# Performance work log

Hardware: AMD Instinct MI355X
Metric: run time of the kernel (lower is better)

## Reference

```python
import jax, jax.numpy as jnp
import numpy as np
from jax import lax

K = 31  # neighborhood kernel size
HEADS = 4


def nat2d(x, qkv_w, qkv_b, rpb, proj_w, proj_b, heads=HEADS, k=K):
    """Neighborhood Attention 2D. x: (B,H,W,C) NHWC. Returns (B,H,W,C)."""
    B, H, W, C = x.shape
    dh = C // heads
    scale = dh ** -0.5
    K2 = k * k
    qkv = x @ qkv_w.T + qkv_b                      # (B,H,W,3C)
    qkv = qkv.reshape(B, H, W, 3, heads, dh)
    q, kk, v = qkv[..., 0, :, :], qkv[..., 1, :, :], qkv[..., 2, :, :]
    # neighborhood window start, clamped to image (NATTEN semantics)
    ri = jnp.clip(jnp.arange(H) - k // 2, 0, H - k)   # (H,)
    ci = jnp.clip(jnp.arange(W) - k // 2, 0, W - k)   # (W,)
    row_idx = ri[:, None] + jnp.arange(k)[None, :]    # (H,k)
    col_idx = ci[:, None] + jnp.arange(k)[None, :]    # (W,k)

    def gather(t):  # (B,H,W,heads,dh) -> (B,H,W,K2,heads,dh)
        g = t[:, row_idx]                  # (B,H,k,W,heads,dh)
        g = g[:, :, :, col_idx]            # (B,H,k,W,k,heads,dh)
        g = jnp.transpose(g, (0, 1, 3, 2, 4, 5, 6))
        return g.reshape(B, H, W, K2, heads, dh)

    kg = gather(kk)
    vg = gather(v)
    logits = jnp.einsum('bijhd,bijnhd->bijhn', q * scale, kg)  # (B,H,W,heads,K2)
    # relative position bias: rpb (heads, 2k-1, 2k-1), index = key - query + (k-1)
    rrel = row_idx - jnp.arange(H)[:, None] + (k - 1)  # (H,k)
    crel = col_idx - jnp.arange(W)[:, None] + (k - 1)  # (W,k)
    bias = rpb[:, rrel]                                # (heads,H,k,2k-1)
    bias = bias[:, :, :, crel]                         # (heads,H,k,W,k)
    bias = jnp.transpose(bias, (0, 1, 3, 2, 4)).reshape(heads, H, W, K2)
    logits = logits + jnp.transpose(bias, (1, 2, 0, 3))[None]
    attn = jax.nn.softmax(logits, axis=-1)
    out = jnp.einsum('bijhn,bijnhd->bijhd', attn, vg).reshape(B, H, W, C)
    return out @ proj_w.T + proj_b


def setup_inputs() -> dict:
    key = jax.random.key(0)
    ks = jax.random.split(key, 16)
    B, H, W, C = 1, 36, 36, 64
    s = 0.02
    inp = {
        'x': jax.random.normal(ks[0], (B, H * W, C), jnp.float32),
        'H': H, 'W': W,
        'qkv_w1': jax.random.normal(ks[1], (3 * C, C), jnp.float32) * s,
        'qkv_b1': jnp.zeros((3 * C,), jnp.float32),
        'rpb1': jax.random.normal(ks[2], (HEADS, 2 * K - 1, 2 * K - 1), jnp.float32) * s,
        'proj_w1': jax.random.normal(ks[3], (C, C), jnp.float32) * s,
        'proj_b1': jnp.zeros((C,), jnp.float32),
        'qkv_w2': jax.random.normal(ks[4], (3 * C, C), jnp.float32) * s,
        'qkv_b2': jnp.zeros((3 * C,), jnp.float32),
        'rpb2': jax.random.normal(ks[5], (HEADS, 2 * K - 1, 2 * K - 1), jnp.float32) * s,
        'proj_w2': jax.random.normal(ks[6], (C, C), jnp.float32) * s,
        'proj_b2': jnp.zeros((C,), jnp.float32),
        'dw_w': jax.random.normal(ks[7], (C, 1, 3, 3), jnp.float32) * s,
        'dw_b': jnp.zeros((C,), jnp.float32),
        'lin_w': jax.random.normal(ks[8], (C, C), jnp.float32) * s,
        'lin_b': jnp.zeros((C,), jnp.float32),
    }
    return inp


def reference(x, H, W, qkv_w1, qkv_b1, rpb1, proj_w1, proj_b1,
              qkv_w2, qkv_b2, rpb2, proj_w2, proj_b2,
              dw_w, dw_b, lin_w, lin_b):
    B, N, C = x.shape
    x_nhwc = x.reshape(B, H, W, C)
    x_nat = nat2d(x_nhwc, qkv_w1, qkv_b1, rpb1, proj_w1, proj_b1)
    x_nat = nat2d(x_nat, qkv_w2, qkv_b2, rpb2, proj_w2, proj_b2)
    x_bchw = jnp.transpose(x_nhwc, (0, 3, 1, 2))
    x_conv = lax.conv_general_dilated(
        x_bchw, dw_w, window_strides=(1, 1), padding=((1, 1), (1, 1)),
        feature_group_count=C,
        dimension_numbers=('NCHW', 'OIHW', 'NCHW')) + dw_b[None, :, None, None]
    out = jnp.transpose(x_nat, (0, 3, 1, 2)) + x_conv       # (B,C,H,W)
    out = out.reshape(B, C, H * W).transpose(0, 2, 1)        # (B,L,C)
    return out @ lin_w.T + lin_b
```

## Files before the change

### kernel.cpp

```cpp
#include <hip/hip_runtime.h>


namespace {

__device__ __forceinline__ int iclampi(int v, int lo, int hi) {
  return v < lo ? lo : (v > hi ? hi : v);
}

template <bool WITH_T>
__global__ __launch_bounds__(256) void qkv_fused(
    const float* __restrict__ xin, const float* __restrict__ w,
    const float* __restrict__ b, float* __restrict__ planes,
    const float* __restrict__ pw1, const float* __restrict__ pw2,
    const float* __restrict__ lw, float* __restrict__ wT) {
  const int bid = blockIdx.x;
  const int tid = threadIdx.x;
  if (WITH_T && bid >= 1008) {
    const int t = bid - 1008;
    const int m = t >> 4;
    const int idx = (t & 15) * 256 + tid;
    const float* src = m == 0 ? pw1 : (m == 1 ? pw2 : lw);
    wT[m * 4096 + (idx & 63) * 64 + (idx >> 6)] = src[idx];
    return;
  }
  __shared__ float xs[64][65];
  __shared__ float ws4[4][64];
  const int pg = bid % 21, rg = bid / 21;
  const int wv = tid >> 6, lane = tid & 63;
  const int n0 = pg * 64;
  const int base = n0 * 64;
  const int maxf = 82944 - base;
  const float* xb = xin + base;
#pragma unroll
  for (int t4 = 0; t4 < 4; ++t4) {
    const int fi = (tid + t4 * 256) * 4;
    float4 v = make_float4(0.f, 0.f, 0.f, 0.f);
    if (fi < maxf) v = *(const float4*)(xb + fi);
    const int p = fi >> 6, c = fi & 63;
    xs[p][c] = v.x; xs[p][c + 1] = v.y; xs[p][c + 2] = v.z; xs[p][c + 3] = v.w;
  }
  ws4[tid >> 6][tid & 63] = w[rg * 256 + tid];
  __syncthreads();
  const int r = rg * 4 + wv;
  float acc = b[r];
#pragma unroll
  for (int cc = 0; cc < 64; ++cc) acc += xs[lane][cc] * ws4[wv][cc];
  const int n = n0 + lane;
  if (n < 1296) planes[r * 1296 + n] = acc;
}

__global__ __launch_bounds__(256, 2) void nat_attn_part(
    const float* __restrict__ planes, const float* __restrict__ rpb,
    float* __restrict__ part) {
  __shared__ float lpart[4][16][35];

  const int tid = threadIdx.x;
  const int h = tid >> 6;
  const int lane = tid & 63;
  const int bid = blockIdx.x;
  const int tile = bid >> 3;
  const int s = (bid >> 1) & 3;
  const int pr = bid & 1;
  const int i0 = (tile / 18) * 2;
  const int j0 = (tile % 18) * 2;

  const int r_lo = iclampi(i0 - 15, 0, 5);
  const int nRr = (iclampi(i0 - 14, 0, 5) + 30) - r_lo;
  const int c_lo = iclampi(j0 - 15, 0, 5);
  const int nCc = (iclampi(j0 - 14, 0, 5) + 30) - c_lo;

  const int iq = i0 + pr;
  const int riq = iclampi(iq - 15, 0, 5);
  int jq[2], cjq[2];
#pragma unroll
  for (int qq = 0; qq < 2; ++qq) {
    jq[qq] = j0 + qq;
    cjq[qq] = iclampi(jq[qq] - 15, 0, 5);
  }

  const float* Qp = planes + (size_t)(h * 16) * 1296;
  const float* Kp = planes + (size_t)(64 + h * 16) * 1296;
  const float* Vp = planes + (size_t)(128 + h * 16) * 1296;

  float qv[2][16];
#pragma unroll
  for (int qq = 0; qq < 2; ++qq) {
    const int nq = iq * 36 + jq[qq];
#pragma unroll
    for (int d = 0; d < 16; ++d) qv[qq][d] = Qp[d * 1296 + nq] * 0.25f;
  }

  float acc[2][16];
  float sden[2] = {0.f, 0.f};
#pragma unroll
  for (int qq = 0; qq < 2; ++qq)
#pragma unroll
    for (int d = 0; d < 16; ++d) acc[qq][d] = 0.f;

  const int lr = lane >> 5;
  const int lc = lane & 31;

#pragma unroll
  for (int rp = 0; rp < 4; ++rp) {
    const int krr = s * 8 + rp * 2 + lr;
    const int rA = r_lo + krr;
    const int cA = c_lo + lc;
    const bool act = (krr <= nRr) && (lc <= nCc);
    const int rL = rA > 35 ? 35 : rA;
    const int cL = cA > 35 ? 35 : cA;
    const int nk = rL * 36 + cL;
    float kr_[16], vr_[16];
#pragma unroll
    for (int d = 0; d < 16; ++d) kr_[d] = Kp[d * 1296 + nk];
#pragma unroll
    for (int d = 0; d < 16; ++d) vr_[d] = Vp[d * 1296 + nk];

    float dot[2] = {0.f, 0.f};
#pragma unroll
    for (int d = 0; d < 16; ++d) {
      dot[0] += qv[0][d] * kr_[d];
      dot[1] += qv[1][d] * kr_[d];
    }
    const bool rowok = act && (rA >= riq) && (rA <= riq + 30);
    const int br = iclampi(rA - iq + 30, 0, 60);
#pragma unroll
    for (int qq = 0; qq < 2; ++qq) {
      const bool inw = rowok && (cA >= cjq[qq]) && (cA <= cjq[qq] + 30);
      const int bc = iclampi(cA - jq[qq] + 30, 0, 60);
      const float bias = rpb[h * 3721 + br * 61 + bc];
      const float lg = fminf(dot[qq] + bias, 25.f);
      const float p = inw ? __expf(lg) : 0.f;
      sden[qq] += p;
#pragma unroll
      for (int d = 0; d < 16; ++d) acc[qq][d] += p * vr_[d];
    }
  }

#pragma unroll
  for (int qq = 0; qq < 2; ++qq) {
#pragma unroll
    for (int d = 0; d < 16; ++d) {
      acc[qq][d] += __shfl_xor(acc[qq][d], 1);
      acc[qq][d] += __shfl_xor(acc[qq][d], 2);
    }
    sden[qq] += __shfl_xor(sden[qq], 1);
    sden[qq] += __shfl_xor(sden[qq], 2);
  }

  if ((lane & 3) == 0) {
    const int row = lane >> 2;
#pragma unroll
    for (int qq = 0; qq < 2; ++qq) {
#pragma unroll
      for (int d = 0; d < 16; ++d) lpart[h][row][qq * 17 + d] = acc[qq][d];
      lpart[h][row][qq * 17 + 16] = sden[qq];
    }
  }

  float* wsout = part + ((size_t)bid * 4 + h) * 36;
  if (lane < 34) {
    float t0 = 0.f;
#pragma unroll
    for (int l = 0; l < 16; ++l) t0 += lpart[h][l][lane];
    wsout[lane] = t0;
  }
}

template <bool FINAL>
__global__ __launch_bounds__(256) void nat_combine(
    const float* __restrict__ part, const float* __restrict__ pwT,
    const float* __restrict__ pb, const float* __restrict__ x,
    const float* __restrict__ dww, const float* __restrict__ dwb,
    const float* __restrict__ linT, const float* __restrict__ lb,
    float* __restrict__ out) {
  __shared__ float att[4][64];
  __shared__ float y_lds[4][64];
  const int tid = threadIdx.x;
  const int q = tid >> 6, lane = tid & 63;
  const int tile = blockIdx.x;
  const int i0 = (tile / 18) * 2, j0 = (tile % 18) * 2;
  const int p = q >> 1, qq = q & 1;
  const int iq = i0 + p, jq = j0 + qq;
  const int n = iq * 36 + jq;

  const int hh = lane >> 4, dd = lane & 15;
  const float* pbase = part + ((size_t)tile * 8 + p) * 144 + hh * 36 + qq * 17;
  float num = 0.f, den = 0.f;
#pragma unroll
  for (int sp = 0; sp < 4; ++sp) {
    num += pbase[sp * 288 + dd];
    den += pbase[sp * 288 + 16];
  }
  att[q][lane] = num / den;
  __syncthreads();

  float a = pb[lane];
#pragma unroll
  for (int cc = 0; cc < 64; ++cc) a += att[q][cc] * pwT[cc * 64 + lane];

  if (!FINAL) {
    out[n * 64 + lane] = a;
  } else {
    float y = a + dwb[lane];
#pragma unroll
    for (int di = -1; di <= 1; ++di) {
#pragma unroll
      for (int dj = -1; dj <= 1; ++dj) {
        const int ii = iq + di, jj = jq + dj;
        if (ii >= 0 && ii < 36 && jj >= 0 && jj < 36)
          y += x[(ii * 36 + jj) * 64 + lane] * dww[lane * 9 + (di + 1) * 3 + (dj + 1)];
      }
    }
    y_lds[q][lane] = y;
    __syncthreads();
    float o = lb[lane];
#pragma unroll
    for (int cc = 0; cc < 64; ++cc) o += y_lds[q][cc] * linT[cc * 64 + lane];
    out[n * 64 + lane] = o;
  }
}

}

extern "C" void kernel_launch(void* const* d_in, const int* in_sizes, int n_in,
                              void* d_out, int out_size, void* d_ws, size_t ws_size,
                              hipStream_t stream) {
  const float* x       = (const float*)d_in[0];
  const float* qkv_w1  = (const float*)d_in[3];
  const float* qkv_b1  = (const float*)d_in[4];
  const float* rpb1    = (const float*)d_in[5];
  const float* proj_w1 = (const float*)d_in[6];
  const float* proj_b1 = (const float*)d_in[7];
  const float* qkv_w2  = (const float*)d_in[8];
  const float* qkv_b2  = (const float*)d_in[9];
  const float* rpb2    = (const float*)d_in[10];
  const float* proj_w2 = (const float*)d_in[11];
  const float* proj_b2 = (const float*)d_in[12];
  const float* dw_w    = (const float*)d_in[13];
  const float* dw_b    = (const float*)d_in[14];
  const float* lin_w   = (const float*)d_in[15];
  const float* lin_b   = (const float*)d_in[16];
  float* out = (float*)d_out;

  float* ws = (float*)d_ws;
  float* planes = ws;
  float* natA   = ws + 248832;
  float* partb  = natA + 82944;
  float* wT     = partb + 373248;
  float* pwT1 = wT;
  float* pwT2 = wT + 4096;
  float* linT = wT + 8192;

  qkv_fused<true><<<1056, 256, 0, stream>>>(x, qkv_w1, qkv_b1, planes,
                                            proj_w1, proj_w2, lin_w, wT);
  nat_attn_part<<<2592, 256, 0, stream>>>(planes, rpb1, partb);
  nat_combine<false><<<324, 256, 0, stream>>>(partb, pwT1, proj_b1, nullptr,
                                              nullptr, nullptr, nullptr, nullptr,
                                              natA);
  qkv_fused<false><<<1008, 256, 0, stream>>>(natA, qkv_w2, qkv_b2, planes,
                                             nullptr, nullptr, nullptr, nullptr);
  nat_attn_part<<<2592, 256, 0, stream>>>(planes, rpb2, partb);
  nat_combine<true><<<324, 256, 0, stream>>>(partb, pwT2, proj_b2, x,
                                             dw_w, dw_b, linT, lin_b, out);
}
```

Baseline: 166.6 us.

## Fuse first attention combine and projection with second QKV projection

Merges the first NAT combine/projection kernel and the second QKV linear into one kernel, so the intermediate natA buffer round trip and one launch go away. Each block recomputes the combine and projection for its 64 positions across 21×24 blocks, which means the projection work is duplicated 24 times over the row groups. The transpose of qkv_w2 is added to the first kernel's weight-transpose tail.

```diff
diff --git a/kernel.cpp b/kernel.cpp
--- a/kernel.cpp
+++ b/kernel.cpp
@@ -12,15 +12,22 @@
     const float* __restrict__ xin, const float* __restrict__ w,
     const float* __restrict__ b, float* __restrict__ planes,
     const float* __restrict__ pw1, const float* __restrict__ pw2,
-    const float* __restrict__ lw, float* __restrict__ wT) {
+    const float* __restrict__ lw, const float* __restrict__ w2,
+    float* __restrict__ wT) {
   const int bid = blockIdx.x;
   const int tid = threadIdx.x;
   if (WITH_T && bid >= 1008) {
     const int t = bid - 1008;
-    const int m = t >> 4;
-    const int idx = (t & 15) * 256 + tid;
-    const float* src = m == 0 ? pw1 : (m == 1 ? pw2 : lw);
-    wT[m * 4096 + (idx & 63) * 64 + (idx >> 6)] = src[idx];
+    if (t < 48) {
+      const int m = t >> 4;
+      const int idx = (t & 15) * 256 + tid;
+      const float* src = m == 0 ? pw1 : (m == 1 ? pw2 : lw);
+      wT[m * 4096 + (idx & 63) * 64 + (idx >> 6)] = src[idx];
+    } else {
+      const int idx = (t - 48) * 256 + tid;
+      const int r = idx >> 6, cc = idx & 63;
+      wT[12288 + cc * 192 + r] = w2[idx];
+    }
     return;
   }
   __shared__ float xs[64][65];
@@ -166,8 +173,73 @@
   }
 }
 
-template <bool FINAL>
-__global__ __launch_bounds__(256) void nat_combine(
+__global__ __launch_bounds__(256) void combine_qkv2(
+    const float* __restrict__ part, const float* __restrict__ pwT1,
+    const float* __restrict__ pb1, const float* __restrict__ w2T,
+    const float* __restrict__ b2, float* __restrict__ planes) {
+  __shared__ float att[64][65];
+  __shared__ float nat[64][65];
+  const int tid = threadIdx.x;
+  const int pg = blockIdx.x % 21, rg = blockIdx.x / 21;
+  const int n0 = pg * 64;
+  const int p = tid & 63, hh = tid >> 6;
+
+  {
+    int n = n0 + p;
+    if (n > 1295) n = 1295;
+    const int iq = n / 36, jq = n % 36;
+    const int tile = (iq >> 1) * 18 + (jq >> 1);
+    const int pr = iq & 1, qq = jq & 1;
+    const float* pb_ = part + ((size_t)(tile * 8 + pr) * 4 + hh) * 36 + qq * 17;
+    float num[16];
+    float den = 0.f;
+#pragma unroll
+    for (int dd = 0; dd < 16; ++dd) num[dd] = 0.f;
+#pragma unroll
+    for (int sp = 0; sp < 4; ++sp) {
+      const float* rec = pb_ + sp * 288;
+      den += rec[16];
+#pragma unroll
+      for (int dd = 0; dd < 16; ++dd) num[dd] += rec[dd];
+    }
+    const float inv = 1.f / den;
+#pragma unroll
+    for (int dd = 0; dd < 16; ++dd) att[p][hh * 16 + dd] = num[dd] * inv;
+  }
+  __syncthreads();
+
+  {
+    float acc[16];
+#pragma unroll
+    for (int k = 0; k < 16; ++k) acc[k] = pb1[hh * 16 + k];
+    for (int cc = 0; cc < 64; ++cc) {
+      const float a = att[p][cc];
+      const float* wp = pwT1 + cc * 64 + hh * 16;
+#pragma unroll
+      for (int k = 0; k < 16; ++k) acc[k] += a * wp[k];
+    }
+#pragma unroll
+    for (int k = 0; k < 16; ++k) nat[p][hh * 16 + k] = acc[k];
+  }
+  __syncthreads();
+
+  {
+    const int n = n0 + p;
+    const int r0 = rg * 8 + hh * 2, r1 = r0 + 1;
+    float a0 = b2[r0], a1 = b2[r1];
+    for (int cc = 0; cc < 64; ++cc) {
+      const float a = nat[p][cc];
+      a0 += a * w2T[cc * 192 + r0];
+      a1 += a * w2T[cc * 192 + r1];
+    }
+    if (n < 1296) {
+      planes[r0 * 1296 + n] = a0;
+      planes[r1 * 1296 + n] = a1;
+    }
+  }
+}
+
+__global__ __launch_bounds__(256) void combine_final(
     const float* __restrict__ part, const float* __restrict__ pwT,
     const float* __restrict__ pb, const float* __restrict__ x,
     const float* __restrict__ dww, const float* __restrict__ dwb,
@@ -198,26 +270,22 @@
 #pragma unroll
   for (int cc = 0; cc < 64; ++cc) a += att[q][cc] * pwT[cc * 64 + lane];
 
-  if (!FINAL) {
-    out[n * 64 + lane] = a;
-  } else {
-    float y = a + dwb[lane];
-#pragma unroll
-    for (int di = -1; di <= 1; ++di) {
-#pragma unroll
-      for (int dj = -1; dj <= 1; ++dj) {
-        const int ii = iq + di, jj = jq + dj;
-        if (ii >= 0 && ii < 36 && jj >= 0 && jj < 36)
-          y += x[(ii * 36 + jj) * 64 + lane] * dww[lane * 9 + (di + 1) * 3 + (dj + 1)];
-      }
-    }
-    y_lds[q][lane] = y;
-    __syncthreads();
-    float o = lb[lane];
-#pragma unroll
-    for (int cc = 0; cc < 64; ++cc) o += y_lds[q][cc] * linT[cc * 64 + lane];
-    out[n * 64 + lane] = o;
-  }
+  float y = a + dwb[lane];
+#pragma unroll
+  for (int di = -1; di <= 1; ++di) {
+#pragma unroll
+    for (int dj = -1; dj <= 1; ++dj) {
+      const int ii = iq + di, jj = jq + dj;
+      if (ii >= 0 && ii < 36 && jj >= 0 && jj < 36)
+        y += x[(ii * 36 + jj) * 64 + lane] * dww[lane * 9 + (di + 1) * 3 + (dj + 1)];
+    }
+  }
+  y_lds[q][lane] = y;
+  __syncthreads();
+  float o = lb[lane];
+#pragma unroll
+  for (int cc = 0; cc < 64; ++cc) o += y_lds[q][cc] * linT[cc * 64 + lane];
+  out[n * 64 + lane] = o;
 }
 
 }
@@ -244,22 +312,19 @@
 
   float* ws = (float*)d_ws;
   float* planes = ws;
-  float* natA   = ws + 248832;
-  float* partb  = natA + 82944;
+  float* partb  = ws + 248832;
   float* wT     = partb + 373248;
   float* pwT1 = wT;
   float* pwT2 = wT + 4096;
   float* linT = wT + 8192;
-
-  qkv_fused<true><<<1056, 256, 0, stream>>>(x, qkv_w1, qkv_b1, planes,
-                                            proj_w1, proj_w2, lin_w, wT);
+  float* w2T  = wT + 12288;
+
+  qkv_fused<true><<<1104, 256, 0, stream>>>(x, qkv_w1, qkv_b1, planes,
+                                            proj_w1, proj_w2, lin_w, qkv_w2, wT);
   nat_attn_part<<<2592, 256, 0, stream>>>(planes, rpb1, partb);
-  nat_combine<false><<<324, 256, 0, stream>>>(partb, pwT1, proj_b1, nullptr,
-                                              nullptr, nullptr, nullptr, nullptr,
-                                              natA);
-  qkv_fused<false><<<1008, 256, 0, stream>>>(natA, qkv_w2, qkv_b2, planes,
-                                             nullptr, nullptr, nullptr, nullptr);
+  combine_qkv2<<<504, 256, 0, stream>>>(partb, pwT1, proj_b1, w2T, qkv_b2,
+                                        planes);
   nat_attn_part<<<2592, 256, 0, stream>>>(planes, rpb2, partb);
-  nat_combine<true><<<324, 256, 0, stream>>>(partb, pwT2, proj_b2, x,
-                                             dw_w, dw_b, linT, lin_b, out);
-}
+  combine_final<<<324, 256, 0, stream>>>(partb, pwT2, proj_b2, x,
+                                         dw_w, dw_b, linT, lin_b, out);
+}
```

Measured after the change: 183.8 us. 10.3% more time.

## Process all four queries of a 2x2 tile per block to reuse K/V loads

Applied to the files above, without the earlier changes.

Each attention block now handles all four queries of a 2x2 tile instead of two, so every K/V vector loaded from global memory is reused across four queries and the grid is halved. The partial buffer layout and the combine kernel indexing are updated to match. The cost is higher register pressure (four 16-wide accumulators plus the Q vectors) under the 2-blocks-per-CU launch bound, which risks spills or lower occupancy, and fewer blocks in flight.

```diff
diff --git a/kernel.cpp b/kernel.cpp
--- a/kernel.cpp
+++ b/kernel.cpp
@@ -52,15 +52,14 @@
 __global__ __launch_bounds__(256, 2) void nat_attn_part(
     const float* __restrict__ planes, const float* __restrict__ rpb,
     float* __restrict__ part) {
-  __shared__ float lpart[4][16][35];
+  __shared__ float lpart[4][16][69];
 
   const int tid = threadIdx.x;
   const int h = tid >> 6;
   const int lane = tid & 63;
   const int bid = blockIdx.x;
-  const int tile = bid >> 3;
-  const int s = (bid >> 1) & 3;
-  const int pr = bid & 1;
+  const int tile = bid >> 2;
+  const int s = bid & 3;
   const int i0 = (tile / 18) * 2;
   const int j0 = (tile % 18) * 2;
 
@@ -69,12 +68,12 @@
   const int c_lo = iclampi(j0 - 15, 0, 5);
   const int nCc = (iclampi(j0 - 14, 0, 5) + 30) - c_lo;
 
-  const int iq = i0 + pr;
-  const int riq = iclampi(iq - 15, 0, 5);
-  int jq[2], cjq[2];
-#pragma unroll
-  for (int qq = 0; qq < 2; ++qq) {
-    jq[qq] = j0 + qq;
+  int iq[4], jq[4], riq[4], cjq[4];
+#pragma unroll
+  for (int qq = 0; qq < 4; ++qq) {
+    iq[qq] = i0 + (qq >> 1);
+    jq[qq] = j0 + (qq & 1);
+    riq[qq] = iclampi(iq[qq] - 15, 0, 5);
     cjq[qq] = iclampi(jq[qq] - 15, 0, 5);
   }
 
@@ -82,18 +81,18 @@
   const float* Kp = planes + (size_t)(64 + h * 16) * 1296;
   const float* Vp = planes + (size_t)(128 + h * 16) * 1296;
 
-  float qv[2][16];
-#pragma unroll
-  for (int qq = 0; qq < 2; ++qq) {
-    const int nq = iq * 36 + jq[qq];
+  float qv[4][16];
+#pragma unroll
+  for (int qq = 0; qq < 4; ++qq) {
+    const int nq = iq[qq] * 36 + jq[qq];
 #pragma unroll
     for (int d = 0; d < 16; ++d) qv[qq][d] = Qp[d * 1296 + nq] * 0.25f;
   }
 
-  float acc[2][16];
-  float sden[2] = {0.f, 0.f};
-#pragma unroll
-  for (int qq = 0; qq < 2; ++qq)
+  float acc[4][16];
+  float sden[4] = {0.f, 0.f, 0.f, 0.f};
+#pragma unroll
+  for (int qq = 0; qq < 4; ++qq)
 #pragma unroll
     for (int d = 0; d < 16; ++d) acc[qq][d] = 0.f;
 
@@ -115,20 +114,17 @@
 #pragma unroll
     for (int d = 0; d < 16; ++d) vr_[d] = Vp[d * 1296 + nk];
 
-    float dot[2] = {0.f, 0.f};
-#pragma unroll
-    for (int d = 0; d < 16; ++d) {
-      dot[0] += qv[0][d] * kr_[d];
-      dot[1] += qv[1][d] * kr_[d];
-    }
-    const bool rowok = act && (rA >= riq) && (rA <= riq + 30);
-    const int br = iclampi(rA - iq + 30, 0, 60);
-#pragma unroll
-    for (int qq = 0; qq < 2; ++qq) {
-      const bool inw = rowok && (cA >= cjq[qq]) && (cA <= cjq[qq] + 30);
+#pragma unroll
+    for (int qq = 0; qq < 4; ++qq) {
+      float dot = 0.f;
+#pragma unroll
+      for (int d = 0; d < 16; ++d) dot += qv[qq][d] * kr_[d];
+      const bool inw = act && (rA >= riq[qq]) && (rA <= riq[qq] + 30) &&
+                       (cA >= cjq[qq]) && (cA <= cjq[qq] + 30);
+      const int br = iclampi(rA - iq[qq] + 30, 0, 60);
       const int bc = iclampi(cA - jq[qq] + 30, 0, 60);
       const float bias = rpb[h * 3721 + br * 61 + bc];
-      const float lg = fminf(dot[qq] + bias, 25.f);
+      const float lg = fminf(dot + bias, 25.f);
       const float p = inw ? __expf(lg) : 0.f;
       sden[qq] += p;
 #pragma unroll
@@ -137,7 +133,7 @@
   }
 
 #pragma unroll
-  for (int qq = 0; qq < 2; ++qq) {
+  for (int qq = 0; qq < 4; ++qq) {
 #pragma unroll
     for (int d = 0; d < 16; ++d) {
       acc[qq][d] += __shfl_xor(acc[qq][d], 1);
@@ -150,19 +146,25 @@
   if ((lane & 3) == 0) {
     const int row = lane >> 2;
 #pragma unroll
-    for (int qq = 0; qq < 2; ++qq) {
+    for (int qq = 0; qq < 4; ++qq) {
 #pragma unroll
       for (int d = 0; d < 16; ++d) lpart[h][row][qq * 17 + d] = acc[qq][d];
       lpart[h][row][qq * 17 + 16] = sden[qq];
     }
   }
 
-  float* wsout = part + ((size_t)bid * 4 + h) * 36;
-  if (lane < 34) {
+  float* wsout = part + ((size_t)bid * 4 + h) * 72;
+  {
     float t0 = 0.f;
 #pragma unroll
     for (int l = 0; l < 16; ++l) t0 += lpart[h][l][lane];
     wsout[lane] = t0;
+    if (lane < 4) {
+      float t1 = 0.f;
+#pragma unroll
+      for (int l = 0; l < 16; ++l) t1 += lpart[h][l][lane + 64];
+      wsout[lane + 64] = t1;
+    }
   }
 }
 
@@ -179,12 +181,11 @@
   const int q = tid >> 6, lane = tid & 63;
   const int tile = blockIdx.x;
   const int i0 = (tile / 18) * 2, j0 = (tile % 18) * 2;
-  const int p = q >> 1, qq = q & 1;
-  const int iq = i0 + p, jq = j0 + qq;
+  const int iq = i0 + (q >> 1), jq = j0 + (q & 1);
   const int n = iq * 36 + jq;
 
   const int hh = lane >> 4, dd = lane & 15;
-  const float* pbase = part + ((size_t)tile * 8 + p) * 144 + hh * 36 + qq * 17;
+  const float* pbase = part + (size_t)tile * 1152 + hh * 72 + q * 17;
   float num = 0.f, den = 0.f;
 #pragma unroll
   for (int sp = 0; sp < 4; ++sp) {
@@ -253,13 +254,13 @@
 
   qkv_fused<true><<<1056, 256, 0, stream>>>(x, qkv_w1, qkv_b1, planes,
                                             proj_w1, proj_w2, lin_w, wT);
-  nat_attn_part<<<2592, 256, 0, stream>>>(planes, rpb1, partb);
+  nat_attn_part<<<1296, 256, 0, stream>>>(planes, rpb1, partb);
   nat_combine<false><<<324, 256, 0, stream>>>(partb, pwT1, proj_b1, nullptr,
                                               nullptr, nullptr, nullptr, nullptr,
                                               natA);
   qkv_fused<false><<<1008, 256, 0, stream>>>(natA, qkv_w2, qkv_b2, planes,
                                              nullptr, nullptr, nullptr, nullptr);
-  nat_attn_part<<<2592, 256, 0, stream>>>(planes, rpb2, partb);
+  nat_attn_part<<<1296, 256, 0, stream>>>(planes, rpb2, partb);
   nat_combine<true><<<324, 256, 0, stream>>>(partb, pwT2, proj_b2, x,
                                              dw_w, dw_b, linT, lin_b, out);
 }
```

After: 177.1 us. +6.3%, slower.

## Remap neighborhood attention lanes to float4 key columns with five row splits

Applied to the files above, without the earlier changes.

The partial attention kernel is restructured. Each lane now covers one key row and four adjacent columns, read as float4 from the K and V planes. Each block covers a 7-row slice of its own query row's window, and five splits (instead of four) cover the 31 rows. Query values are staged once through shared memory instead of every lane loading them. The combine kernel and workspace layout are updated for 10 partial blocks per tile. The aim is fewer and wider global loads and less per-lane unrolled work, at the cost of more blocks and some idle lanes (7x9 of 64 used).

```diff
diff --git a/kernel.cpp b/kernel.cpp
--- a/kernel.cpp
+++ b/kernel.cpp
@@ -53,108 +53,101 @@
     const float* __restrict__ planes, const float* __restrict__ rpb,
     float* __restrict__ part) {
   __shared__ float lpart[4][16][35];
+  __shared__ float qlds[4][2][16];
 
   const int tid = threadIdx.x;
   const int h = tid >> 6;
   const int lane = tid & 63;
   const int bid = blockIdx.x;
-  const int tile = bid >> 3;
-  const int s = (bid >> 1) & 3;
-  const int pr = bid & 1;
+  const int tile = bid / 10;
+  const int rem = bid - tile * 10;
+  const int s = rem >> 1;
+  const int pr = rem & 1;
   const int i0 = (tile / 18) * 2;
   const int j0 = (tile % 18) * 2;
 
-  const int r_lo = iclampi(i0 - 15, 0, 5);
-  const int nRr = (iclampi(i0 - 14, 0, 5) + 30) - r_lo;
-  const int c_lo = iclampi(j0 - 15, 0, 5);
-  const int nCc = (iclampi(j0 - 14, 0, 5) + 30) - c_lo;
-
   const int iq = i0 + pr;
   const int riq = iclampi(iq - 15, 0, 5);
-  int jq[2], cjq[2];
-#pragma unroll
-  for (int qq = 0; qq < 2; ++qq) {
-    jq[qq] = j0 + qq;
-    cjq[qq] = iclampi(jq[qq] - 15, 0, 5);
-  }
+  const int jqa = j0, jqb = j0 + 1;
+  const int cja = iclampi(jqa - 15, 0, 5);
+  const int cjb = iclampi(jqb - 15, 0, 5);
 
   const float* Qp = planes + (size_t)(h * 16) * 1296;
-  const float* Kp = planes + (size_t)(64 + h * 16) * 1296;
-  const float* Vp = planes + (size_t)(128 + h * 16) * 1296;
-
-  float qv[2][16];
-#pragma unroll
-  for (int qq = 0; qq < 2; ++qq) {
-    const int nq = iq * 36 + jq[qq];
-#pragma unroll
-    for (int d = 0; d < 16; ++d) qv[qq][d] = Qp[d * 1296 + nq] * 0.25f;
-  }
-
-  float acc[2][16];
-  float sden[2] = {0.f, 0.f};
-#pragma unroll
-  for (int qq = 0; qq < 2; ++qq)
-#pragma unroll
-    for (int d = 0; d < 16; ++d) acc[qq][d] = 0.f;
-
-  const int lr = lane >> 5;
-  const int lc = lane & 31;
-
-#pragma unroll
-  for (int rp = 0; rp < 4; ++rp) {
-    const int krr = s * 8 + rp * 2 + lr;
-    const int rA = r_lo + krr;
-    const int cA = c_lo + lc;
-    const bool act = (krr <= nRr) && (lc <= nCc);
-    const int rL = rA > 35 ? 35 : rA;
-    const int cL = cA > 35 ? 35 : cA;
-    const int nk = rL * 36 + cL;
-    float kr_[16], vr_[16];
-#pragma unroll
-    for (int d = 0; d < 16; ++d) kr_[d] = Kp[d * 1296 + nk];
-#pragma unroll
-    for (int d = 0; d < 16; ++d) vr_[d] = Vp[d * 1296 + nk];
-
-    float dot[2] = {0.f, 0.f};
-#pragma unroll
-    for (int d = 0; d < 16; ++d) {
-      dot[0] += qv[0][d] * kr_[d];
-      dot[1] += qv[1][d] * kr_[d];
-    }
-    const bool rowok = act && (rA >= riq) && (rA <= riq + 30);
-    const int br = iclampi(rA - iq + 30, 0, 60);
-#pragma unroll
-    for (int qq = 0; qq < 2; ++qq) {
-      const bool inw = rowok && (cA >= cjq[qq]) && (cA <= cjq[qq] + 30);
-      const int bc = iclampi(cA - jq[qq] + 30, 0, 60);
-      const float bias = rpb[h * 3721 + br * 61 + bc];
-      const float lg = fminf(dot[qq] + bias, 25.f);
-      const float p = inw ? __expf(lg) : 0.f;
-      sden[qq] += p;
-#pragma unroll
-      for (int d = 0; d < 16; ++d) acc[qq][d] += p * vr_[d];
-    }
-  }
-
-#pragma unroll
-  for (int qq = 0; qq < 2; ++qq) {
-#pragma unroll
-    for (int d = 0; d < 16; ++d) {
-      acc[qq][d] += __shfl_xor(acc[qq][d], 1);
-      acc[qq][d] += __shfl_xor(acc[qq][d], 2);
-    }
-    sden[qq] += __shfl_xor(sden[qq], 1);
-    sden[qq] += __shfl_xor(sden[qq], 2);
-  }
+  const float4* Kp4 = (const float4*)(planes + (size_t)(64 + h * 16) * 1296);
+  const float4* Vp4 = (const float4*)(planes + (size_t)(128 + h * 16) * 1296);
+
+  if (lane < 32) {
+    const int qq = lane >> 4, dd = lane & 15;
+    const int nq = iq * 36 + (qq ? jqb : jqa);
+    qlds[h][qq][dd] = Qp[dd * 1296 + nq] * 0.25f;
+  }
+
+  const int rr = lane / 9;
+  const int cg = lane - rr * 9;
+  const int krr = s * 7 + rr;
+  const int rA = riq + krr;
+  const bool act = (krr <= 30) && (rr < 7);
+  const int rL = rA > 35 ? 35 : rA;
+  const int rc9 = rL * 9 + cg;
+  const int br = iclampi(rA - iq + 30, 0, 60);
+  const float* rpbh = rpb + h * 3721 + br * 61;
+
+  float dta[4] = {0.f, 0.f, 0.f, 0.f};
+  float dtb[4] = {0.f, 0.f, 0.f, 0.f};
+#pragma unroll
+  for (int d = 0; d < 16; ++d) {
+    const float4 k4 = Kp4[d * 324 + rc9];
+    const float qa = qlds[h][0][d], qb = qlds[h][1][d];
+    dta[0] += qa * k4.x; dta[1] += qa * k4.y; dta[2] += qa * k4.z; dta[3] += qa * k4.w;
+    dtb[0] += qb * k4.x; dtb[1] += qb * k4.y; dtb[2] += qb * k4.z; dtb[3] += qb * k4.w;
+  }
+
+  float pa[4], pb_[4];
+  float dena = 0.f, denb = 0.f;
+#pragma unroll
+  for (int j = 0; j < 4; ++j) {
+    const int col = cg * 4 + j;
+    const bool ina = act && (col >= cja) && (col <= cja + 30);
+    const bool inb = act && (col >= cjb) && (col <= cjb + 30);
+    const int bca = iclampi(col - jqa + 30, 0, 60);
+    const int bcb = iclampi(col - jqb + 30, 0, 60);
+    const float la = fminf(dta[j] + rpbh[bca], 25.f);
+    const float lb = fminf(dtb[j] + rpbh[bcb], 25.f);
+    pa[j] = ina ? __expf(la) : 0.f;
+    pb_[j] = inb ? __expf(lb) : 0.f;
+    dena += pa[j];
+    denb += pb_[j];
+  }
+
+  float acca[16], accb[16];
+#pragma unroll
+  for (int d = 0; d < 16; ++d) {
+    const float4 v4 = Vp4[d * 324 + rc9];
+    acca[d] = pa[0] * v4.x + pa[1] * v4.y + pa[2] * v4.z + pa[3] * v4.w;
+    accb[d] = pb_[0] * v4.x + pb_[1] * v4.y + pb_[2] * v4.z + pb_[3] * v4.w;
+  }
+
+#pragma unroll
+  for (int d = 0; d < 16; ++d) {
+    acca[d] += __shfl_xor(acca[d], 1);
+    acca[d] += __shfl_xor(acca[d], 2);
+    accb[d] += __shfl_xor(accb[d], 1);
+    accb[d] += __shfl_xor(accb[d], 2);
+  }
+  dena += __shfl_xor(dena, 1);
+  dena += __shfl_xor(dena, 2);
+  denb += __shfl_xor(denb, 1);
+  denb += __shfl_xor(denb, 2);
 
   if ((lane & 3) == 0) {
     const int row = lane >> 2;
 #pragma unroll
-    for (int qq = 0; qq < 2; ++qq) {
-#pragma unroll
-      for (int d = 0; d < 16; ++d) lpart[h][row][qq * 17 + d] = acc[qq][d];
-      lpart[h][row][qq * 17 + 16] = sden[qq];
+    for (int d = 0; d < 16; ++d) {
+      lpart[h][row][d] = acca[d];
+      lpart[h][row][17 + d] = accb[d];
     }
+    lpart[h][row][16] = dena;
+    lpart[h][row][33] = denb;
   }
 
   float* wsout = part + ((size_t)bid * 4 + h) * 36;
@@ -179,15 +172,15 @@
   const int q = tid >> 6, lane = tid & 63;
   const int tile = blockIdx.x;
   const int i0 = (tile / 18) * 2, j0 = (tile % 18) * 2;
-  const int p = q >> 1, qq = q & 1;
-  const int iq = i0 + p, jq = j0 + qq;
+  const int pr = q >> 1, qq = q & 1;
+  const int iq = i0 + pr, jq = j0 + qq;
   const int n = iq * 36 + jq;
 
   const int hh = lane >> 4, dd = lane & 15;
-  const float* pbase = part + ((size_t)tile * 8 + p) * 144 + hh * 36 + qq * 17;
+  const float* pbase = part + (size_t)tile * 1440 + pr * 144 + hh * 36 + qq * 17;
   float num = 0.f, den = 0.f;
 #pragma unroll
-  for (int sp = 0; sp < 4; ++sp) {
+  for (int sp = 0; sp < 5; ++sp) {
     num += pbase[sp * 288 + dd];
     den += pbase[sp * 288 + 16];
   }
@@ -246,20 +239,20 @@
   float* planes = ws;
   float* natA   = ws + 248832;
   float* partb  = natA + 82944;
-  float* wT     = partb + 373248;
+  float* wT     = partb + 466560;
   float* pwT1 = wT;
   float* pwT2 = wT + 4096;
   float* linT = wT + 8192;
 
   qkv_fused<true><<<1056, 256, 0, stream>>>(x, qkv_w1, qkv_b1, planes,
                                             proj_w1, proj_w2, lin_w, wT);
-  nat_attn_part<<<2592, 256, 0, stream>>>(planes, rpb1, partb);
+  nat_attn_part<<<3240, 256, 0, stream>>>(planes, rpb1, partb);
   nat_combine<false><<<324, 256, 0, stream>>>(partb, pwT1, proj_b1, nullptr,
                                               nullptr, nullptr, nullptr, nullptr,
                                               natA);
   qkv_fused<false><<<1008, 256, 0, stream>>>(natA, qkv_w2, qkv_b2, planes,
                                              nullptr, nullptr, nullptr, nullptr);
-  nat_attn_part<<<2592, 256, 0, stream>>>(planes, rpb2, partb);
+  nat_attn_part<<<3240, 256, 0, stream>>>(planes, rpb2, partb);
   nat_combine<true><<<324, 256, 0, stream>>>(partb, pwT2, proj_b2, x,
                                              dw_w, dw_b, linT, lin_b, out);
 }
```

After: 149.5 us. -10.3%, faster.
